# Performance work log

Measured on AMD Instinct MI355X. Metric: run time of the kernel, lower is better.

## Reference

```python
import jax, jax.numpy as jnp
import numpy as np

B, M, N, C = 8192, 16, 256, 64


def setup_inputs() -> dict:
    key = jax.random.key(0)
    k1, k2 = jax.random.split(key)
    inputs = jax.random.normal(k1, (B, M, C), dtype=jnp.float32)
    codebook = jax.random.normal(k2, (M, N, C), dtype=jnp.float32)
    return {"inputs": inputs, "codebook": codebook}


def reference(inputs, codebook):
    # inputs: [B, M, C]; codebook: [M, N, C]
    # (avoids materializing the torch [B, M, N, C] broadcast difference)
    x2 = jnp.sum(inputs * inputs, axis=-1)[:, :, None]          # [B, M, 1]
    c2 = jnp.sum(codebook * codebook, axis=-1)[None, :, :]      # [1, M, N]
    xc = jnp.einsum('bmc,mnc->bmn', inputs, codebook)           # [B, M, N]
    dist = x2 - 2.0 * xc + c2                                   # [B, M, N]
    idx = jnp.argmin(dist, axis=-1)                             # [B, M] int
    m_idx = jnp.arange(codebook.shape[0])[None, :]              # [1, M]
    codes = codebook[m_idx, idx]                                # [B, M, C]
    return codes, idx
```

## Files before the change

kernel.cpp:

```cpp
#include <hip/hip_runtime.h>
#include <hip/hip_bf16.h>
#include <float.h>


#define BQ 8192
#define MQ 16
#define NQ 256
#define CQ 64
#define RPB 512
#define NTILES 8

typedef short  shortx8 __attribute__((ext_vector_type(8)));
typedef float  f32x4   __attribute__((ext_vector_type(4)));

#define HI_MASK 0xffff0000u

__device__ __forceinline__ void split3_pair(float a, float b,
                                            uint& q0, uint& q1, uint& q2) {
    const uint ba = __builtin_bit_cast(uint, a);
    const uint bb = __builtin_bit_cast(uint, b);
    q0 = (ba >> 16) | (bb & HI_MASK);
    const float r1a = a - __builtin_bit_cast(float, ba & HI_MASK);
    const float r1b = b - __builtin_bit_cast(float, bb & HI_MASK);
    const uint c1a = __builtin_bit_cast(uint, r1a);
    const uint c1b = __builtin_bit_cast(uint, r1b);
    q1 = (c1a >> 16) | (c1b & HI_MASK);
    const float r2a = r1a - __builtin_bit_cast(float, c1a & HI_MASK);
    const float r2b = r1b - __builtin_bit_cast(float, c1b & HI_MASK);
    q2 = (__builtin_bit_cast(uint, r2a) >> 16) |
         (__builtin_bit_cast(uint, r2b) & HI_MASK);
}

__device__ __forceinline__ void fq_stage(const float* __restrict__ inputs,
        int row0, int m, float* buf, int w, int lane) {
    #pragma unroll
    for (int i = 0; i < 2; ++i) {
        const int blk = i * 8 + w;
        const int f   = (blk << 6) + lane;
        const int r   = f >> 4;
        const int c   = (f & 15) ^ (r & 7);
        const float* src = inputs + ((size_t)(row0 + r) * MQ + m) * CQ + (c << 2);
        __builtin_amdgcn_global_load_lds(
            (const __attribute__((address_space(1))) void*)src,
            (__attribute__((address_space(3))) void*)(buf + (blk << 8)),
            16, 0, 0);
    }
}

__global__ __launch_bounds__(512, 2) void fq_fused_kernel(
        const float* __restrict__ inputs,
        const float* __restrict__ codebook,
        float* __restrict__ out_codes,
        float* __restrict__ out_idx) {
    const int m    = blockIdx.y;
    const int rowB = blockIdx.x * RPB;
    const int w    = (int)threadIdx.x >> 6;
    const int lane = (int)threadIdx.x & 63;
    const int quad = lane >> 4;
    const int col  = lane & 15;
    const int rw   = w & 3;
    const int chh  = w >> 2;

    __shared__ unsigned short lds_b[96 * 512];
    __shared__ float sx[2][64][64];
    __shared__ float s_c2v[NQ];
    __shared__ float s_wb[2][64];
    __shared__ int   s_wi[2][64];
    __shared__ int   s_win[64];

    fq_stage(inputs, rowB,      m, &sx[0][0][0], w, lane);
    fq_stage(inputs, rowB + 64, m, &sx[1][0][0], w, lane);

    const float* cbm = codebook + (size_t)m * NQ * CQ;
    #pragma unroll
    for (int it = 0; it < 4; ++it) {
        const int item = (int)threadIdx.x + it * 512;
        const int kc = item & 7;
        const int n  = item >> 3;
        const int nt = n >> 4, cc = n & 15;
        const int h = kc >> 2, q = kc & 3;
        const float* src = cbm + (size_t)n * CQ + kc * 8;
        const float4 va = *(const float4*)src;
        const float4 vb = *(const float4*)(src + 4);
        const float el[8] = {va.x, va.y, va.z, va.w, vb.x, vb.y, vb.z, vb.w};

        float s = 0.0f;
        #pragma unroll
        for (int u = 0; u < 8; ++u) s = fmaf(el[u], el[u], s);
        s += __shfl_xor(s, 1, 64);
        s += __shfl_xor(s, 2, 64);
        s += __shfl_xor(s, 4, 64);
        if (kc == 0) s_c2v[n] = s;

        uint p0[4], p1[4], p2[4];
        #pragma unroll
        for (int u = 0; u < 4; ++u)
            split3_pair(el[2 * u], el[2 * u + 1], p0[u], p1[u], p2[u]);
        const int lf = q * 16 + cc;
        #pragma unroll
        for (int j = 0; j < 3; ++j) {
            const uint* p = (j == 0) ? p0 : (j == 1) ? p1 : p2;
            unsigned short* dst =
                &lds_b[(((j << 1) + h) * 16 + nt) * 512 + lf * 8];
            *(uint4*)dst = make_uint4(p[0], p[1], p[2], p[3]);
        }
    }
    __syncthreads();

    float c2r[8];
    #pragma unroll
    for (int nt = 0; nt < 8; ++nt)
        c2r[nt] = s_c2v[chh * 128 + nt * 16 + col];

    #pragma unroll 1
    for (int t = 0; t < NTILES; ++t) {
        const int row0 = rowB + t * 64;
        const float* sxb = &sx[t & 1][0][0];

        shortx8 afr[3][2];
        const int r = rw * 16 + col;
        const float* rowp = sxb + r * 64;
        #pragma unroll
        for (int h = 0; h < 2; ++h) {
            const int p0i = (h * 8 + quad * 2) ^ (r & 7);
            const float4 va = *(const float4*)(rowp + (p0i << 2));
            const float4 vb = *(const float4*)(rowp + ((p0i ^ 1) << 2));
            const float el[8] = {va.x, va.y, va.z, va.w, vb.x, vb.y, vb.z, vb.w};
            uint q0[4], q1[4], q2[4];
            #pragma unroll
            for (int u = 0; u < 4; ++u)
                split3_pair(el[2 * u], el[2 * u + 1], q0[u], q1[u], q2[u]);
            afr[0][h] = __builtin_bit_cast(shortx8,
                make_uint4(q0[0], q0[1], q0[2], q0[3]));
            afr[1][h] = __builtin_bit_cast(shortx8,
                make_uint4(q1[0], q1[1], q1[2], q1[3]));
            afr[2][h] = __builtin_bit_cast(shortx8,
                make_uint4(q2[0], q2[1], q2[2], q2[3]));
        }

        f32x4 acc[8];
        #pragma unroll
        for (int nt = 0; nt < 8; ++nt)
            acc[nt] = (f32x4){0.f, 0.f, 0.f, 0.f};

        #pragma unroll
        for (int h = 0; h < 2; ++h) {
            #pragma unroll
            for (int j = 0; j < 3; ++j) {
                shortx8 bfr[8];
                #pragma unroll
                for (int nt = 0; nt < 8; ++nt)
                    bfr[nt] = *(const shortx8*)
                        &lds_b[(((j << 1) + h) * 16 + chh * 8 + nt) * 512
                               + lane * 8];
                #pragma unroll
                for (int i = 0; i <= 2 - j; ++i) {
                    #pragma unroll
                    for (int nt = 0; nt < 8; ++nt)
                        acc[nt] = __builtin_amdgcn_mfma_f32_16x16x32_bf16(
                            afr[i][h], bfr[nt], acc[nt], 0, 0, 0);
                }
            }
        }

        #pragma unroll
        for (int reg = 0; reg < 4; ++reg) {
            float bd = FLT_MAX; int bi = 0;
            #pragma unroll
            for (int nt = 0; nt < 8; ++nt) {
                const float d = fmaf(-2.0f, acc[nt][reg], c2r[nt]);
                if (d < bd) { bd = d; bi = chh * 128 + nt * 16 + col; }
            }
            #pragma unroll
            for (int mask = 1; mask <= 8; mask <<= 1) {
                const float od = __shfl_xor(bd, mask, 64);
                const int   oi = __shfl_xor(bi, mask, 64);
                if (od < bd || (od == bd && oi < bi)) { bd = od; bi = oi; }
            }
            if (col == 0) {
                const int rr = rw * 16 + quad * 4 + reg;
                s_wb[chh][rr] = bd;
                s_wi[chh][rr] = bi;
            }
        }
        __syncthreads();

        if (w == 0) {
            float bd = s_wb[0][lane]; int bi = s_wi[0][lane];
            const float od = s_wb[1][lane]; const int oi = s_wi[1][lane];
            if (od < bd || (od == bd && oi < bi)) { bd = od; bi = oi; }
            s_win[lane] = bi;
            out_idx[(size_t)(row0 + lane) * MQ + m] = (float)bi;
        }
        __syncthreads();

        if (t + 2 < NTILES)
            fq_stage(inputs, row0 + 128, m, &sx[t & 1][0][0], w, lane);

        #pragma unroll 4
        for (int jj = 0; jj < 8; ++jj) {
            const int rr = w * 8 + jj;
            const int bn = s_win[rr];
            out_codes[((size_t)(row0 + rr) * MQ + m) * CQ + lane] =
                cbm[(size_t)bn * CQ + lane];
        }
    }
}

extern "C" void kernel_launch(void* const* d_in, const int* in_sizes, int n_in,
                              void* d_out, int out_size, void* d_ws, size_t ws_size,
                              hipStream_t stream) {
    const float* inputs   = (const float*)d_in[0];
    const float* codebook = (const float*)d_in[1];
    float* out_codes = (float*)d_out;
    float* out_idx   = (float*)d_out + (size_t)BQ * MQ * CQ;
    (void)d_ws; (void)ws_size;

    fq_fused_kernel<<<dim3(BQ / RPB, MQ), 512, 0, stream>>>(
        inputs, codebook, out_codes, out_idx);
}
```

Baseline: 116.8 us.

## Give each wave its own rows with direct global loads and in-register argmin

The block grows to 1024 threads, and each wave now owns 32 rows, processed as two 16-row tiles. Each wave loops over both codebook halves itself instead of splitting them across waves. A-operands are read straight from global memory rather than staged into LDS with async loads, and the cross-wave argmin through shared memory plus its two barriers per tile are removed. This trades a sequential chh loop per wave and unpipelined global loads for less synchronisation, less LDS use, and more waves in flight.

```diff
diff --git a/kernel.cpp b/kernel.cpp
--- a/kernel.cpp
+++ b/kernel.cpp
@@ -8,7 +8,6 @@
 #define NQ 256
 #define CQ 64
 #define RPB 512
-#define NTILES 8
 
 typedef short  shortx8 __attribute__((ext_vector_type(8)));
 typedef float  f32x4   __attribute__((ext_vector_type(4)));
@@ -31,23 +30,7 @@
          (__builtin_bit_cast(uint, r2b) & HI_MASK);
 }
 
-__device__ __forceinline__ void fq_stage(const float* __restrict__ inputs,
-        int row0, int m, float* buf, int w, int lane) {
-    #pragma unroll
-    for (int i = 0; i < 2; ++i) {
-        const int blk = i * 8 + w;
-        const int f   = (blk << 6) + lane;
-        const int r   = f >> 4;
-        const int c   = (f & 15) ^ (r & 7);
-        const float* src = inputs + ((size_t)(row0 + r) * MQ + m) * CQ + (c << 2);
-        __builtin_amdgcn_global_load_lds(
-            (const __attribute__((address_space(1))) void*)src,
-            (__attribute__((address_space(3))) void*)(buf + (blk << 8)),
-            16, 0, 0);
-    }
-}
-
-__global__ __launch_bounds__(512, 2) void fq_fused_kernel(
+__global__ __launch_bounds__(1024, 4) void fq_fused_kernel(
         const float* __restrict__ inputs,
         const float* __restrict__ codebook,
         float* __restrict__ out_codes,
@@ -58,23 +41,14 @@
     const int lane = (int)threadIdx.x & 63;
     const int quad = lane >> 4;
     const int col  = lane & 15;
-    const int rw   = w & 3;
-    const int chh  = w >> 2;
 
     __shared__ unsigned short lds_b[96 * 512];
-    __shared__ float sx[2][64][64];
     __shared__ float s_c2v[NQ];
-    __shared__ float s_wb[2][64];
-    __shared__ int   s_wi[2][64];
-    __shared__ int   s_win[64];
-
-    fq_stage(inputs, rowB,      m, &sx[0][0][0], w, lane);
-    fq_stage(inputs, rowB + 64, m, &sx[1][0][0], w, lane);
 
     const float* cbm = codebook + (size_t)m * NQ * CQ;
     #pragma unroll
-    for (int it = 0; it < 4; ++it) {
-        const int item = (int)threadIdx.x + it * 512;
+    for (int it = 0; it < 2; ++it) {
+        const int item = (int)threadIdx.x + it * 1024;
         const int kc = item & 7;
         const int n  = item >> 3;
         const int nt = n >> 4, cc = n & 15;
@@ -107,24 +81,16 @@
     }
     __syncthreads();
 
-    float c2r[8];
-    #pragma unroll
-    for (int nt = 0; nt < 8; ++nt)
-        c2r[nt] = s_c2v[chh * 128 + nt * 16 + col];
+    #pragma unroll 1
+    for (int tt = 0; tt < 2; ++tt) {
+        const int row0 = rowB + w * 32 + tt * 16;
 
-    #pragma unroll 1
-    for (int t = 0; t < NTILES; ++t) {
-        const int row0 = rowB + t * 64;
-        const float* sxb = &sx[t & 1][0][0];
-
+        const float* xb = inputs + ((size_t)(row0 + col) * MQ + m) * CQ;
         shortx8 afr[3][2];
-        const int r = rw * 16 + col;
-        const float* rowp = sxb + r * 64;
         #pragma unroll
         for (int h = 0; h < 2; ++h) {
-            const int p0i = (h * 8 + quad * 2) ^ (r & 7);
-            const float4 va = *(const float4*)(rowp + (p0i << 2));
-            const float4 vb = *(const float4*)(rowp + ((p0i ^ 1) << 2));
+            const float4 va = *(const float4*)(xb + h * 32 + quad * 8);
+            const float4 vb = *(const float4*)(xb + h * 32 + quad * 8 + 4);
             const float el[8] = {va.x, va.y, va.z, va.w, vb.x, vb.y, vb.z, vb.w};
             uint q0[4], q1[4], q2[4];
             #pragma unroll
@@ -138,70 +104,73 @@
                 make_uint4(q2[0], q2[1], q2[2], q2[3]));
         }
 
-        f32x4 acc[8];
-        #pragma unroll
-        for (int nt = 0; nt < 8; ++nt)
-            acc[nt] = (f32x4){0.f, 0.f, 0.f, 0.f};
+        float bd0[4]; int bi0[4];
+        #pragma unroll 1
+        for (int chh = 0; chh < 2; ++chh) {
+            float c2r[8];
+            #pragma unroll
+            for (int nt = 0; nt < 8; ++nt)
+                c2r[nt] = s_c2v[chh * 128 + nt * 16 + col];
 
-        #pragma unroll
-        for (int h = 0; h < 2; ++h) {
+            f32x4 acc[8];
             #pragma unroll
-            for (int j = 0; j < 3; ++j) {
-                shortx8 bfr[8];
+            for (int nt = 0; nt < 8; ++nt)
+                acc[nt] = (f32x4){0.f, 0.f, 0.f, 0.f};
+
+            #pragma unroll
+            for (int h = 0; h < 2; ++h) {
                 #pragma unroll
-                for (int nt = 0; nt < 8; ++nt)
-                    bfr[nt] = *(const shortx8*)
-                        &lds_b[(((j << 1) + h) * 16 + chh * 8 + nt) * 512
-                               + lane * 8];
-                #pragma unroll
-                for (int i = 0; i <= 2 - j; ++i) {
+                for (int j = 0; j < 3; ++j) {
+                    shortx8 bfr[8];
                     #pragma unroll
                     for (int nt = 0; nt < 8; ++nt)
-                        acc[nt] = __builtin_amdgcn_mfma_f32_16x16x32_bf16(
-                            afr[i][h], bfr[nt], acc[nt], 0, 0, 0);
+                        bfr[nt] = *(const shortx8*)
+                            &lds_b[(((j << 1) + h) * 16 + chh * 8 + nt) * 512
+                                   + lane * 8];
+                    #pragma unroll
+                    for (int i = 0; i <= 2 - j; ++i) {
+                        #pragma unroll
+                        for (int nt = 0; nt < 8; ++nt)
+                            acc[nt] = __builtin_amdgcn_mfma_f32_16x16x32_bf16(
+                                afr[i][h], bfr[nt], acc[nt], 0, 0, 0);
+                    }
+                }
+            }
+
+            #pragma unroll
+            for (int reg = 0; reg < 4; ++reg) {
+                float bd = FLT_MAX; int bi = 0;
+                #pragma unroll
+                for (int nt = 0; nt < 8; ++nt) {
+                    const float d = fmaf(-2.0f, acc[nt][reg], c2r[nt]);
+                    if (d < bd) { bd = d; bi = chh * 128 + nt * 16 + col; }
+                }
+                #pragma unroll
+                for (int mask = 1; mask <= 8; mask <<= 1) {
+                    const float od = __shfl_xor(bd, mask, 64);
+                    const int   oi = __shfl_xor(bi, mask, 64);
+                    if (od < bd || (od == bd && oi < bi)) { bd = od; bi = oi; }
+                }
+                if (chh == 0) { bd0[reg] = bd; bi0[reg] = bi; }
+                else {
+                    if (bd < bd0[reg] || (bd == bd0[reg] && bi < bi0[reg])) {
+                        bd0[reg] = bd; bi0[reg] = bi;
+                    }
                 }
             }
         }
 
+        if (col == 0) {
+            #pragma unroll
+            for (int reg = 0; reg < 4; ++reg)
+                out_idx[(size_t)(row0 + quad * 4 + reg) * MQ + m] =
+                    (float)bi0[reg];
+        }
+
         #pragma unroll
-        for (int reg = 0; reg < 4; ++reg) {
-            float bd = FLT_MAX; int bi = 0;
-            #pragma unroll
-            for (int nt = 0; nt < 8; ++nt) {
-                const float d = fmaf(-2.0f, acc[nt][reg], c2r[nt]);
-                if (d < bd) { bd = d; bi = chh * 128 + nt * 16 + col; }
-            }
-            #pragma unroll
-            for (int mask = 1; mask <= 8; mask <<= 1) {
-                const float od = __shfl_xor(bd, mask, 64);
-                const int   oi = __shfl_xor(bi, mask, 64);
-                if (od < bd || (od == bd && oi < bi)) { bd = od; bi = oi; }
-            }
-            if (col == 0) {
-                const int rr = rw * 16 + quad * 4 + reg;
-                s_wb[chh][rr] = bd;
-                s_wi[chh][rr] = bi;
-            }
-        }
-        __syncthreads();
-
-        if (w == 0) {
-            float bd = s_wb[0][lane]; int bi = s_wi[0][lane];
-            const float od = s_wb[1][lane]; const int oi = s_wi[1][lane];
-            if (od < bd || (od == bd && oi < bi)) { bd = od; bi = oi; }
-            s_win[lane] = bi;
-            out_idx[(size_t)(row0 + lane) * MQ + m] = (float)bi;
-        }
-        __syncthreads();
-
-        if (t + 2 < NTILES)
-            fq_stage(inputs, row0 + 128, m, &sx[t & 1][0][0], w, lane);
-
-        #pragma unroll 4
-        for (int jj = 0; jj < 8; ++jj) {
-            const int rr = w * 8 + jj;
-            const int bn = s_win[rr];
-            out_codes[((size_t)(row0 + rr) * MQ + m) * CQ + lane] =
+        for (int jj = 0; jj < 16; ++jj) {
+            const int bn = __shfl(bi0[jj & 3], (jj >> 2) * 16, 64);
+            out_codes[((size_t)(row0 + jj) * MQ + m) * CQ + lane] =
                 cbm[(size_t)bn * CQ + lane];
         }
     }
@@ -216,6 +185,6 @@
     float* out_idx   = (float*)d_out + (size_t)BQ * MQ * CQ;
     (void)d_ws; (void)ws_size;
 
-    fq_fused_kernel<<<dim3(BQ / RPB, MQ), 512, 0, stream>>>(
+    fq_fused_kernel<<<dim3(BQ / RPB, MQ), 1024, 0, stream>>>(
         inputs, codebook, out_codes, out_idx);
 }
```

After: 108.1 us. 1.08x faster.
